# Kernel optimization log

Measured on AMD Instinct MI355X. Metric: run time of the kernel, lower is better.

The kernel has to match this reference:

```python
import jax, jax.numpy as jnp
import numpy as np

NUM_GRAPHS = 128
EPS = 1e-5


def _instance_norm(x, seg):
    # per-graph (segment) normalization over rows, per channel; affine=False (PyG default)
    ones = jnp.ones((x.shape[0],), x.dtype)
    cnt = jnp.maximum(jax.ops.segment_sum(ones, seg, num_segments=NUM_GRAPHS), 1.0)[:, None]
    mean = jax.ops.segment_sum(x, seg, num_segments=NUM_GRAPHS) / cnt
    ex2 = jax.ops.segment_sum(x * x, seg, num_segments=NUM_GRAPHS) / cnt
    var = jnp.maximum(ex2 - mean * mean, 0.0)
    return (x - mean[seg]) * jax.lax.rsqrt(var[seg] + EPS)


def setup_inputs() -> dict:
    key = jax.random.key(0)
    ks = jax.random.split(key, 6)
    N, E, H = 100_000, 1_600_000, 64
    emb = jax.random.normal(ks[0], (N, H), jnp.float32)
    edge_index = jax.random.randint(ks[1], (2, E), 0, N)
    batch = jnp.sort(jax.random.randint(ks[2], (N,), 0, NUM_GRAPHS))
    s = lambda fan: 1.0 / np.sqrt(fan)
    # MLP layers [2H, 4H, H, 1]
    W1 = jax.random.uniform(ks[3], (2 * H, 4 * H), jnp.float32, -s(2 * H), s(2 * H))
    b1 = jnp.zeros((4 * H,), jnp.float32)
    W2 = jax.random.uniform(ks[4], (4 * H, H), jnp.float32, -s(4 * H), s(4 * H))
    b2 = jnp.zeros((H,), jnp.float32)
    W3 = jax.random.uniform(ks[5], (H, 1), jnp.float32, -s(H), s(H))
    b3 = jnp.zeros((1,), jnp.float32)
    return dict(emb=emb, edge_index=edge_index, batch=batch,
                W1=W1, b1=b1, W2=W2, b2=b2, W3=W3, b3=b3)


def reference(emb, edge_index, batch, W1, b1, W2, b2, W3, b3):
    col, row = edge_index[0], edge_index[1]
    # edge-wise gather + concat: [E, 2H]
    f12 = jnp.concatenate([emb[col], emb[row]], axis=-1)
    seg = batch[col]  # graph id per edge
    h = jax.nn.relu(_instance_norm(f12 @ W1 + b1, seg))   # [E, 4H]
    h = jax.nn.relu(_instance_norm(h @ W2 + b2, seg))     # [E, H]
    att_log_logits = h @ W3 + b3                          # [E, 1]
    return att_log_logits
```

## Files before the change

kernel.cpp:

```cpp
#include <hip/hip_runtime.h>
#include <hip/hip_bf16.h>

#define NSEG 128
#define H64 64
#define C1 256
#define K1 128
#define C2 64
#define EPSV 1e-5f
#define NWG 256

typedef __attribute__((ext_vector_type(8))) short bf16x8;
typedef __attribute__((ext_vector_type(16))) float f32x16;
typedef __attribute__((ext_vector_type(4))) unsigned int u32x4;

struct BTrue  { static constexpr bool value = true; };
struct BFalse { static constexpr bool value = false; };

__device__ __forceinline__ unsigned short f2bf(float f){
  unsigned int x = __float_as_uint(f);
  x += 0x7fffu + ((x >> 16) & 1u);
  return (unsigned short)(x >> 16);
}
__device__ __forceinline__ float bf2f(unsigned short u){
  return __uint_as_float(((unsigned int)u) << 16);
}
__device__ __forceinline__ unsigned pkbf(float lo, float hi){
  unsigned r;
  asm("v_cvt_pk_bf16_f32 %0, %1, %2" : "=v"(r) : "v"(lo), "v"(hi));
  return r;
}
__device__ __forceinline__ bf16x8 mk8(unsigned a, unsigned b, unsigned c, unsigned d){
  u32x4 t = {a, b, c, d};
  return __builtin_bit_cast(bf16x8, t);
}
__device__ __forceinline__ int xcd_swz(int bid, int nwg){
  int q = nwg >> 3, r = nwg & 7;
  int x = bid & 7, o = bid >> 3;
  return (x < r ? x * (q + 1) : r * (q + 1) + (x - r) * q) + o;
}

__global__ void k_cvt_emb(const float* __restrict__ src, unsigned short* __restrict__ dst, int n4){
  int i = blockIdx.x * blockDim.x + threadIdx.x;
  if (i >= n4) return;
  float4 v = ((const float4*)src)[i];
  unsigned int a = (unsigned int)f2bf(v.x) | ((unsigned int)f2bf(v.y) << 16);
  unsigned int b = (unsigned int)f2bf(v.z) | ((unsigned int)f2bf(v.w) << 16);
  ((uint2*)dst)[i] = make_uint2(a, b);
}

__global__ void k_cvt_w(const float* __restrict__ W1, const float* __restrict__ W2,
                        unsigned short* __restrict__ W1T, unsigned short* __restrict__ W2T){
  int i = blockIdx.x * blockDim.x + threadIdx.x;
  if (i < C1 * K1){
    int c = i >> 7, k = i & 127;
    W1T[i] = f2bf(W1[k * C1 + c]);
  } else {
    int j = i - C1 * K1;
    if (j < C2 * C1){
      int c = j >> 8, k = j & 255;
      W2T[j] = f2bf(W2[k * C2 + c]);
    }
  }
}

__global__ void k_hist(const int* __restrict__ col, const int* __restrict__ batch,
                       int* __restrict__ segE, int* __restrict__ cnt, int E){
  __shared__ int h[NSEG];
  for (int i = threadIdx.x; i < NSEG; i += blockDim.x) h[i] = 0;
  __syncthreads();
  int stride = gridDim.x * blockDim.x;
  for (int e = blockIdx.x * blockDim.x + threadIdx.x; e < E; e += stride){
    int s = batch[col[e]];
    segE[e] = s;
    atomicAdd(&h[s], 1);
  }
  __syncthreads();
  for (int i = threadIdx.x; i < NSEG; i += blockDim.x)
    if (h[i]) atomicAdd(&cnt[i], h[i]);
}

__global__ void k_scan(const int* __restrict__ cnt, int* __restrict__ cursor,
                       float* __restrict__ cntf){
  if (threadIdx.x == 0){
    int acc = 0;
    for (int i = 0; i < NSEG; i++){ cursor[i] = acc; acc += cnt[i]; }
  }
  if (threadIdx.x < NSEG){
    int c = cnt[threadIdx.x];
    cntf[threadIdx.x] = (float)(c > 0 ? c : 1);
  }
}

__global__ void k_scatter(const int* __restrict__ segE, const int* __restrict__ ei,
                          int* __restrict__ cursor, int* __restrict__ perm,
                          int* __restrict__ segS, int* __restrict__ ecol, int* __restrict__ erow,
                          int E, int epb){
  __shared__ int h[NSEG];
  __shared__ int base[NSEG];
  int b0 = blockIdx.x * epb;
  int b1 = b0 + epb < E ? b0 + epb : E;
  for (int i = threadIdx.x; i < NSEG; i += blockDim.x) h[i] = 0;
  __syncthreads();
  for (int e = b0 + threadIdx.x; e < b1; e += blockDim.x) atomicAdd(&h[segE[e]], 1);
  __syncthreads();
  for (int i = threadIdx.x; i < NSEG; i += blockDim.x)
    base[i] = h[i] ? atomicAdd(&cursor[i], h[i]) : 0;
  __syncthreads();
  for (int i = threadIdx.x; i < NSEG; i += blockDim.x) h[i] = 0;
  __syncthreads();
  for (int e = b0 + threadIdx.x; e < b1; e += blockDim.x){
    int s = segE[e];
    int p = base[s] + atomicAdd(&h[s], 1);
    perm[p] = e; segS[p] = s;
    ecol[p] = ei[e]; erow[p] = ei[(size_t)E + e];
  }
}

__global__ void __launch_bounds__(1024, 4)
k_stats1(const unsigned short* __restrict__ ebf, const unsigned short* __restrict__ W1T,
         const int* __restrict__ ecol, const int* __restrict__ erow, const int* __restrict__ segS,
         float* __restrict__ sum1, float* __restrict__ sq1, int NWT, int E, int T)
{
  __shared__ __align__(16) char wl[65536];
  {
    #pragma unroll
    for (int j = 0; j < 4; j++){
      int i = threadIdx.x + j * 1024;
      int r = i >> 4, u = i & 15;
      u32x4 v = *(const u32x4*)(W1T + (size_t)r * K1 + u * 8);
      *(u32x4*)(wl + r * 256 + ((u ^ (r & 15)) << 4)) = v;
    }
  }
  __syncthreads();

  const int lane = threadIdx.x & 63, w = threadIdx.x >> 6;
  const int g = lane >> 5, l31 = lane & 31;
  const int bid = xcd_swz(blockIdx.x, NWG);
  const int wt0 = (bid * 16 + w) * T;
  float psum[8] = {0,0,0,0,0,0,0,0}, psq[8] = {0,0,0,0,0,0,0,0};
  int cur = -1;

  auto flush = [&](int seg){
    if (seg < 0) return;
    #pragma unroll
    for (int nt = 0; nt < 8; nt++){
      float sv = psum[nt] + __shfl_xor(psum[nt], 32);
      float qv = psq[nt]  + __shfl_xor(psq[nt], 32);
      if (lane < 32){
        atomicAdd(&sum1[seg * C1 + nt * 32 + l31], sv);
        atomicAdd(&sq1 [seg * C1 + nt * 32 + l31], qv);
      }
      psum[nt] = 0.f; psq[nt] = 0.f;
    }
  };

  auto ld3 = [&](int wt, int& a, int& r, int& s){
    int e = wt * 32 + l31;
    int ec = e < E ? e : E - 1;
    a = ecol[ec]; r = erow[ec]; s = segS[ec];
  };

  int cA, rA, sg;
  if (wt0 < NWT) ld3(wt0, cA, rA, sg);

  for (int it = 0; it < T; ++it){
    int wt = wt0 + it;
    if (wt >= NWT) break;
    const int p0 = wt * 32;
    int nA, nR, nS;
    const bool hv = (it + 1 < T) && (wt + 1 < NWT);
    if (hv) ld3(wt + 1, nA, nR, nS);

    bf16x8 fa[8];
    #pragma unroll
    for (int kk = 0; kk < 8; kk++){
      int off = (kk & 3) * 16 + g * 8;
      fa[kk] = *(const bf16x8*)(ebf + (size_t)(kk < 4 ? cA : rA) * H64 + off);
    }

    int sA = __builtin_amdgcn_readfirstlane(__shfl(sg, 0));
    int sB = __builtin_amdgcn_readfirstlane(__shfl(sg, 31));
    bool uni = (sA == sB) && (p0 + 32 <= E);
    if (uni && sA != cur){ flush(cur); cur = sA; }
    if (!uni){ flush(cur); cur = -1; }

    #pragma unroll 1
    for (int np = 0; np < 4; np++){
      const int nt0 = 2 * np, nt1 = 2 * np + 1;
      f32x16 a0, a1;
      #pragma unroll
      for (int r = 0; r < 16; r++){ a0[r] = 0.f; a1[r] = 0.f; }
      const int rw0 = nt0 * 32 + l31, rw1 = nt1 * 32 + l31;
      __builtin_amdgcn_s_setprio(1);
      #pragma unroll
      for (int kk = 0; kk < 8; kk++){
        bf16x8 b0 = *(const bf16x8*)(wl + rw0 * 256 + (((2 * kk + g) ^ (rw0 & 15)) << 4));
        bf16x8 b1 = *(const bf16x8*)(wl + rw1 * 256 + (((2 * kk + g) ^ (rw1 & 15)) << 4));
        a0 = __builtin_amdgcn_mfma_f32_32x32x16_bf16(fa[kk], b0, a0, 0, 0, 0);
        a1 = __builtin_amdgcn_mfma_f32_32x32x16_bf16(fa[kk], b1, a1, 0, 0, 0);
      }
      __builtin_amdgcn_s_setprio(0);
      if (uni){
        float t0 = 0.f, q0 = 0.f, t1 = 0.f, q1 = 0.f;
        #pragma unroll
        for (int r = 0; r < 16; r++){
          t0 += a0[r]; q0 += a0[r] * a0[r];
          t1 += a1[r]; q1 += a1[r] * a1[r];
        }
        psum[nt0] += t0; psq[nt0] += q0;
        psum[nt1] += t1; psq[nt1] += q1;
      } else {
        for (int s = sA; s <= sB; s++){
          float t0 = 0.f, q0 = 0.f, t1 = 0.f, q1 = 0.f;
          #pragma unroll
          for (int r = 0; r < 16; r++){
            int c = (r & 3) + 8 * (r >> 2) + 4 * g;
            bool ok = (__shfl(sg, c) == s) && (p0 + c < E);
            float v0 = ok ? a0[r] : 0.f;
            float v1 = ok ? a1[r] : 0.f;
            t0 += v0; q0 += v0 * v0;
            t1 += v1; q1 += v1 * v1;
          }
          float s0 = t0 + __shfl_xor(t0, 32);
          float qq0 = q0 + __shfl_xor(q0, 32);
          float s1 = t1 + __shfl_xor(t1, 32);
          float qq1 = q1 + __shfl_xor(q1, 32);
          if (lane < 32){
            atomicAdd(&sum1[s * C1 + nt0 * 32 + l31], s0);
            atomicAdd(&sq1 [s * C1 + nt0 * 32 + l31], qq0);
            atomicAdd(&sum1[s * C1 + nt1 * 32 + l31], s1);
            atomicAdd(&sq1 [s * C1 + nt1 * 32 + l31], qq1);
          }
        }
      }
    }
    if (hv){ cA = nA; rA = nR; sg = nS; }
  }
  flush(cur);
}

__global__ void k_fin(const float* __restrict__ sum, const float* __restrict__ sq,
                      const float* __restrict__ cntf,
                      float* __restrict__ sc, float* __restrict__ sh, int C){
  int i = blockIdx.x * blockDim.x + threadIdx.x;
  if (i >= NSEG * C) return;
  int s = i / C;
  float c = cntf[s];
  float m = sum[i] / c;
  float v = fmaxf(sq[i] / c - m * m, 0.f);
  float inv = rsqrtf(v + EPSV);
  sc[i] = inv;
  sh[i] = -m * inv;
}

template<int MODE>
__global__ void __launch_bounds__(1024, 4)
k_mid(const unsigned short* __restrict__ ebf, const unsigned short* __restrict__ W1T,
      const unsigned short* __restrict__ W2T,
      const int* __restrict__ ecol, const int* __restrict__ erow,
      const int* __restrict__ segS, const int* __restrict__ perm,
      const float* __restrict__ sc1, const float* __restrict__ sh1,
      float* __restrict__ sum2, float* __restrict__ sq2,
      unsigned int* __restrict__ y2u,
      const float* __restrict__ sc2, const float* __restrict__ sh2,
      const float* __restrict__ W3, const float* __restrict__ b3,
      float* __restrict__ out, int NWT, int E, int T)
{
  __shared__ __align__(16) char wl[98304];
  __shared__ __align__(16) float scsh[16][512];
  {
    #pragma unroll
    for (int j = 0; j < 4; j++){
      int i = threadIdx.x + j * 1024;
      int r = i >> 4, u = i & 15;
      u32x4 v = *(const u32x4*)(W1T + (size_t)r * K1 + u * 8);
      *(u32x4*)(wl + r * 256 + ((u ^ (r & 15)) << 4)) = v;
    }
    #pragma unroll
    for (int j = 0; j < 2; j++){
      int i = threadIdx.x + j * 1024;
      int r = i >> 5, u = i & 31;
      u32x4 v = *(const u32x4*)(W2T + (size_t)r * C1 + u * 8);
      *(u32x4*)(wl + 65536 + r * 512 + ((u ^ (r & 31)) << 4)) = v;
    }
  }
  __syncthreads();

  const int lane = threadIdx.x & 63, w = threadIdx.x >> 6;
  const int g = lane >> 5, l31 = lane & 31;
  const int bid = xcd_swz(blockIdx.x, NWG);
  const int wt0 = (bid * 16 + w) * T;

  float b3v = 0.f;
  if (MODE == 2) b3v = b3[0];
  int wseg = -1;

  auto body = [&](auto uni_c, const bf16x8* fbp, int sgn, f32x16* acc2){
    constexpr bool UNI = decltype(uni_c)::value;
    #pragma unroll 1
    for (int mt = 0; mt < 8; mt++){
      f32x16 a1;
      #pragma unroll
      for (int r = 0; r < 16; r++) a1[r] = 0.f;
      const int rw = mt * 32 + l31;
      __builtin_amdgcn_s_setprio(1);
      #pragma unroll
      for (int kk = 0; kk < 8; kk++){
        bf16x8 wa = *(const bf16x8*)(wl + rw * 256 + (((2 * kk + g) ^ (rw & 15)) << 4));
        a1 = __builtin_amdgcn_mfma_f32_32x32x16_bf16(wa, fbp[kk], a1, 0, 0, 0);
      }
      __builtin_amdgcn_s_setprio(0);
      unsigned pk_[8];
      #pragma unroll
      for (int rq = 0; rq < 4; rq++){
        float4 sc, sh;
        if constexpr (UNI){
          sc = *(const float4*)(&scsh[w][mt * 32 + rq * 8 + 4 * g]);
          sh = *(const float4*)(&scsh[w][256 + mt * 32 + rq * 8 + 4 * g]);
        } else {
          sc = *(const float4*)(sc1 + sgn * C1 + mt * 32 + rq * 8 + 4 * g);
          sh = *(const float4*)(sh1 + sgn * C1 + mt * 32 + rq * 8 + 4 * g);
        }
        float h0 = fmaxf(fmaf(a1[rq * 4 + 0], sc.x, sh.x), 0.f);
        float h1 = fmaxf(fmaf(a1[rq * 4 + 1], sc.y, sh.y), 0.f);
        float h2 = fmaxf(fmaf(a1[rq * 4 + 2], sc.z, sh.z), 0.f);
        float h3 = fmaxf(fmaf(a1[rq * 4 + 3], sc.w, sh.w), 0.f);
        pk_[rq * 2 + 0] = pkbf(h0, h1);
        pk_[rq * 2 + 1] = pkbf(h2, h3);
      }
      asm("v_permlane32_swap_b32 %0, %1" : "+v"(pk_[0]), "+v"(pk_[2]));
      asm("v_permlane32_swap_b32 %0, %1" : "+v"(pk_[1]), "+v"(pk_[3]));
      asm("v_permlane32_swap_b32 %0, %1" : "+v"(pk_[4]), "+v"(pk_[6]));
      asm("v_permlane32_swap_b32 %0, %1" : "+v"(pk_[5]), "+v"(pk_[7]));
      bf16x8 bf0 = mk8(pk_[0], pk_[1], pk_[2], pk_[3]);
      bf16x8 bf1 = mk8(pk_[4], pk_[5], pk_[6], pk_[7]);
      __builtin_amdgcn_s_setprio(1);
      #pragma unroll
      for (int ct = 0; ct < 2; ct++){
        int rb = ct * 32 + l31;
        bf16x8 wb0 = *(const bf16x8*)(wl + 65536 + rb * 512 + (((4 * mt + g) ^ (rb & 31)) << 4));
        bf16x8 wb1 = *(const bf16x8*)(wl + 65536 + rb * 512 + (((4 * mt + 2 + g) ^ (rb & 31)) << 4));
        acc2[ct] = __builtin_amdgcn_mfma_f32_32x32x16_bf16(wb0, bf0, acc2[ct], 0, 0, 0);
        acc2[ct] = __builtin_amdgcn_mfma_f32_32x32x16_bf16(wb1, bf1, acc2[ct], 0, 0, 0);
      }
      __builtin_amdgcn_s_setprio(0);
    }
  };

  auto ld3 = [&](int wt, int& a, int& r, int& s){
    int e = wt * 32 + l31;
    int ec = e < E ? e : E - 1;
    a = ecol[ec]; r = erow[ec]; s = segS[ec];
  };

  int cA, rA, sg;
  if (wt0 < NWT) ld3(wt0, cA, rA, sg);

  for (int it = 0; it < T; ++it){
    int wt = wt0 + it;
    if (wt >= NWT) break;
    const int p0 = wt * 32;
    int nA, nR, nS;
    const bool hv = (it + 1 < T) && (wt + 1 < NWT);
    if (hv) ld3(wt + 1, nA, nR, nS);

    int e0 = p0 + l31;
    bool v0 = e0 < E;

    bf16x8 fb[8];
    #pragma unroll
    for (int kk = 0; kk < 8; kk++){
      int off = (kk & 3) * 16 + g * 8;
      fb[kk] = *(const bf16x8*)(ebf + (size_t)(kk < 4 ? cA : rA) * H64 + off);
    }

    int sA = __builtin_amdgcn_readfirstlane(__shfl(sg, 0));
    int sB = __builtin_amdgcn_readfirstlane(__shfl(sg, 31));
    const bool uni = (sA == sB) && (p0 + 32 <= E);

    if (uni && sA != wseg){
      float4 s4 = *(const float4*)(sc1 + sA * C1 + lane * 4);
      float4 h4 = *(const float4*)(sh1 + sA * C1 + lane * 4);
      *(float4*)(&scsh[w][lane * 4]) = s4;
      *(float4*)(&scsh[w][256 + lane * 4]) = h4;
      wseg = sA;
    }

    f32x16 acc2[2];
    #pragma unroll
    for (int ct = 0; ct < 2; ct++)
      #pragma unroll
      for (int r = 0; r < 16; r++) acc2[ct][r] = 0.f;

    if (uni) body(BTrue{},  fb, sg, acc2);
    else     body(BFalse{}, fb, sg, acc2);

    if constexpr (MODE == 0){
      if (v0){
        unsigned* yp = y2u + (size_t)e0 * 32;
        #pragma unroll
        for (int ct = 0; ct < 2; ct++)
          #pragma unroll
          for (int rq = 0; rq < 4; rq++){
            uint2 pv;
            pv.x = pkbf(acc2[ct][rq * 4 + 0], acc2[ct][rq * 4 + 1]);
            pv.y = pkbf(acc2[ct][rq * 4 + 2], acc2[ct][rq * 4 + 3]);
            *(uint2*)(yp + ct * 16 + rq * 4 + 2 * g) = pv;
          }
      }
    } else if constexpr (MODE == 1){
      for (int s = sA; s <= sB; s++){
        #pragma unroll
        for (int ct = 0; ct < 2; ct++)
          #pragma unroll
          for (int r = 0; r < 16; r++){
            float x = (v0 && sg == s) ? acc2[ct][r] : 0.f;
            float vs = x, vq = x * x;
            #pragma unroll
            for (int off = 1; off < 32; off <<= 1){
              vs += __shfl_xor(vs, off);
              vq += __shfl_xor(vq, off);
            }
            if (l31 == 0){
              int c2 = ct * 32 + (r & 3) + 8 * (r >> 2) + 4 * g;
              atomicAdd(&sum2[s * C2 + c2], vs);
              atomicAdd(&sq2 [s * C2 + c2], vq);
            }
          }
      }
    } else {
      float acc = 0.f;
      #pragma unroll
      for (int ct = 0; ct < 2; ct++)
        #pragma unroll
        for (int rq = 0; rq < 4; rq++){
          float4 sc = *(const float4*)(sc2 + sg * C2 + ct * 32 + rq * 8 + 4 * g);
          float4 sh = *(const float4*)(sh2 + sg * C2 + ct * 32 + rq * 8 + 4 * g);
          float4 wq = *(const float4*)(W3 + ct * 32 + rq * 8 + 4 * g);
          acc = fmaf(fmaxf(fmaf(acc2[ct][rq * 4 + 0], sc.x, sh.x), 0.f), wq.x, acc);
          acc = fmaf(fmaxf(fmaf(acc2[ct][rq * 4 + 1], sc.y, sh.y), 0.f), wq.y, acc);
          acc = fmaf(fmaxf(fmaf(acc2[ct][rq * 4 + 2], sc.z, sh.z), 0.f), wq.z, acc);
          acc = fmaf(fmaxf(fmaf(acc2[ct][rq * 4 + 3], sc.w, sh.w), 0.f), wq.w, acc);
        }
      acc += __shfl_xor(acc, 32);
      if (g == 0 && v0) out[perm[e0]] = acc + b3v;
    }
    if (hv){ cA = nA; rA = nR; sg = nS; }
  }
}

__global__ void k_stats2(const unsigned int* __restrict__ y2u, const int* __restrict__ segS,
                         float* __restrict__ sum2, float* __restrict__ sq2, int E)
{
  const int cp = threadIdx.x & 31;
  const int es = threadIdx.x >> 5;
  int chunk = (E + gridDim.x - 1) / gridDim.x;
  int eb = blockIdx.x * chunk;
  int ee = eb + chunk < E ? eb + chunk : E;
  float s0 = 0.f, s1 = 0.f, q0 = 0.f, q1 = 0.f;
  int cur = -1;
  for (int e = eb + es; e < ee; e += 8){
    int sg = segS[e];
    unsigned v = y2u[(size_t)e * 32 + cp];
    float f0 = bf2f((unsigned short)(v & 0xffff));
    float f1 = bf2f((unsigned short)(v >> 16));
    if (sg != cur){
      if (cur >= 0){
        atomicAdd(&sum2[cur * C2 + 2 * cp], s0);
        atomicAdd(&sum2[cur * C2 + 2 * cp + 1], s1);
        atomicAdd(&sq2 [cur * C2 + 2 * cp], q0);
        atomicAdd(&sq2 [cur * C2 + 2 * cp + 1], q1);
      }
      s0 = s1 = q0 = q1 = 0.f; cur = sg;
    }
    s0 += f0; s1 += f1; q0 += f0 * f0; q1 += f1 * f1;
  }
  if (cur >= 0){
    atomicAdd(&sum2[cur * C2 + 2 * cp], s0);
    atomicAdd(&sum2[cur * C2 + 2 * cp + 1], s1);
    atomicAdd(&sq2 [cur * C2 + 2 * cp], q0);
    atomicAdd(&sq2 [cur * C2 + 2 * cp + 1], q1);
  }
}

__global__ void k_out(const unsigned short* __restrict__ y2, const int* __restrict__ segS,
                      const int* __restrict__ perm, const float* __restrict__ sc2,
                      const float* __restrict__ sh2, const float* __restrict__ W3,
                      const float* __restrict__ b3, float* __restrict__ out, int E)
{
  const int lane = threadIdx.x & 63;
  const int wid = (blockIdx.x * blockDim.x + threadIdx.x) >> 6;
  const int nw = (gridDim.x * blockDim.x) >> 6;
  const int es = lane >> 3;
  const int cp = (lane & 7) * 8;
  float w3r[8];
  #pragma unroll
  for (int j = 0; j < 8; j++) w3r[j] = W3[cp + j];
  const float b3v = b3[0];
  for (long base = (long)wid * 8; base < E; base += (long)nw * 8){
    int pos = (int)base + es;
    float a = 0.f;
    if (pos < E){
      bf16x8 v = *(const bf16x8*)(y2 + (size_t)pos * C2 + cp);
      int s = segS[pos];
      const float* scp = sc2 + s * C2 + cp;
      const float* shp = sh2 + s * C2 + cp;
      #pragma unroll
      for (int j = 0; j < 8; j++){
        float hv = fmaxf(fmaf(bf2f((unsigned short)v[j]), scp[j], shp[j]), 0.f);
        a = fmaf(hv, w3r[j], a);
      }
    }
    a += __shfl_xor(a, 1); a += __shfl_xor(a, 2); a += __shfl_xor(a, 4);
    if ((lane & 7) == 0 && pos < E) out[perm[pos]] = a + b3v;
  }
}

extern "C" void kernel_launch(void* const* d_in, const int* in_sizes, int n_in,
                              void* d_out, int out_size, void* d_ws, size_t ws_size,
                              hipStream_t stream)
{
  const float* emb   = (const float*)d_in[0];
  const int*   ei    = (const int*)d_in[1];
  const int*   batch = (const int*)d_in[2];
  const float* W1    = (const float*)d_in[3];
  const float* W2    = (const float*)d_in[5];
  const float* W3    = (const float*)d_in[7];
  const float* b3    = (const float*)d_in[8];
  float* out = (float*)d_out;
  const int E = in_sizes[1] / 2;
  const int N = in_sizes[0] / H64;
  const int NWT = (E + 31) / 32;

  char* ws = (char*)d_ws;
  size_t o = 0;
  auto al = [&](size_t b){ size_t r = o; o = (o + b + 255) & ~((size_t)255); return r; };
  size_t o_ebf  = al((size_t)N * H64 * 2);
  size_t o_w1t  = al((size_t)C1 * K1 * 2);
  size_t o_w2t  = al((size_t)C2 * C1 * 2);
  size_t o_perm = al((size_t)E * 4);
  size_t o_segS = al((size_t)E * 4);
  size_t o_ecol = al((size_t)E * 4);
  size_t o_erow = al((size_t)E * 4);
  size_t o_cnt  = al(NSEG * 4);
  size_t o_cur  = al(NSEG * 4);
  size_t o_cntf = al(NSEG * 4);
  size_t o_sum1 = al((size_t)NSEG * C1 * 4);
  size_t o_sq1  = al((size_t)NSEG * C1 * 4);
  size_t o_sum2 = al((size_t)NSEG * C2 * 4);
  size_t o_sq2  = al((size_t)NSEG * C2 * 4);
  size_t o_sc1  = al((size_t)NSEG * C1 * 4);
  size_t o_sh1  = al((size_t)NSEG * C1 * 4);
  size_t o_sc2  = al((size_t)NSEG * C2 * 4);
  size_t o_sh2  = al((size_t)NSEG * C2 * 4);
  size_t o_segE = al((size_t)E * 4);
  size_t o_y2   = o_segE;
  size_t need_full = o_segE + (size_t)E * C2 * 2;
  const bool full = ws_size >= need_full;

  unsigned short* ebf = (unsigned short*)(ws + o_ebf);
  unsigned short* W1T = (unsigned short*)(ws + o_w1t);
  unsigned short* W2T = (unsigned short*)(ws + o_w2t);
  int* perm = (int*)(ws + o_perm);
  int* segS = (int*)(ws + o_segS);
  int* ecol = (int*)(ws + o_ecol);
  int* erow = (int*)(ws + o_erow);
  int* cnt  = (int*)(ws + o_cnt);
  int* curp = (int*)(ws + o_cur);
  float* cntf = (float*)(ws + o_cntf);
  float* sum1 = (float*)(ws + o_sum1);
  float* sq1  = (float*)(ws + o_sq1);
  float* sum2 = (float*)(ws + o_sum2);
  float* sq2  = (float*)(ws + o_sq2);
  float* sc1  = (float*)(ws + o_sc1);
  float* sh1  = (float*)(ws + o_sh1);
  float* sc2  = (float*)(ws + o_sc2);
  float* sh2  = (float*)(ws + o_sh2);
  int* segE = (int*)(ws + o_segE);
  unsigned int* y2u = (unsigned int*)(ws + o_y2);
  unsigned short* y2 = (unsigned short*)(ws + o_y2);

  hipMemsetAsync(ws + o_cnt, 0, o_sc1 - o_cnt, stream);

  k_cvt_emb<<<(N * H64 / 4 + 255) / 256, 256, 0, stream>>>(emb, ebf, N * H64 / 4);
  k_cvt_w<<<192, 256, 0, stream>>>(W1, W2, W1T, W2T);

  k_hist<<<2048, 256, 0, stream>>>(ei, batch, segE, cnt, E);
  k_scan<<<1, 128, 0, stream>>>(cnt, curp, cntf);
  const int epb = 2048;
  k_scatter<<<(E + epb - 1) / epb, 256, 0, stream>>>(segE, ei, curp, perm, segS, ecol, erow, E, epb);

  const int T = (NWT + NWG * 16 - 1) / (NWG * 16);
  k_stats1<<<NWG, 1024, 0, stream>>>(ebf, W1T, ecol, erow, segS, sum1, sq1, NWT, E, T);
  k_fin<<<(NSEG * C1) / 256, 256, 0, stream>>>(sum1, sq1, cntf, sc1, sh1, C1);

  if (full){
    k_mid<0><<<NWG, 1024, 0, stream>>>(ebf, W1T, W2T, ecol, erow, segS, perm,
        sc1, sh1, sum2, sq2, y2u, sc2, sh2, W3, b3, out, NWT, E, T);
    k_stats2<<<512, 256, 0, stream>>>(y2u, segS, sum2, sq2, E);
    k_fin<<<(NSEG * C2) / 256, 256, 0, stream>>>(sum2, sq2, cntf, sc2, sh2, C2);
    k_out<<<1024, 256, 0, stream>>>(y2, segS, perm, sc2, sh2, W3, b3, out, E);
  } else {
    k_mid<1><<<NWG, 1024, 0, stream>>>(ebf, W1T, W2T, ecol, erow, segS, perm,
        sc1, sh1, sum2, sq2, nullptr, sc2, sh2, W3, b3, out, NWT, E, T);
    k_fin<<<(NSEG * C2) / 256, 256, 0, stream>>>(sum2, sq2, cntf, sc2, sh2, C2);
    k_mid<2><<<NWG, 1024, 0, stream>>>(ebf, W1T, W2T, ecol, erow, segS, perm,
        sc1, sh1, sum2, sq2, nullptr, sc2, sh2, W3, b3, out, NWT, E, T);
  }
}
```

Measured before the change: 674.1 us.

## Fuse layer-2 stats into mid kernel and replace scattered output write with gather remap

Removes the separate k_stats2 pass by computing layer-2 sum/sumsq with wave shuffles and atomics inside k_mid<0>, alongside the bf16 y2 store. k_out now writes results in sorted order to a temp buffer, and a new k_remap kernel gathers them back to original edge order using an inverse permutation recorded in k_scatter. This trades a full reread of y2 and a scattered write for more shuffle/atomic work in the main kernel, an extra invp write, and one extra small kernel. Stats are now taken from fp32 accumulators rather than the bf16-rounded values.

```diff
diff --git a/kernel.cpp b/kernel.cpp
--- a/kernel.cpp
+++ b/kernel.cpp
@@ -94,7 +94,7 @@
 __global__ void k_scatter(const int* __restrict__ segE, const int* __restrict__ ei,
                           int* __restrict__ cursor, int* __restrict__ perm,
                           int* __restrict__ segS, int* __restrict__ ecol, int* __restrict__ erow,
-                          int E, int epb){
+                          int* __restrict__ invp, int E, int epb){
   __shared__ int h[NSEG];
   __shared__ int base[NSEG];
   int b0 = blockIdx.x * epb;
@@ -113,6 +113,7 @@
     int p = base[s] + atomicAdd(&h[s], 1);
     perm[p] = e; segS[p] = s;
     ecol[p] = ei[e]; erow[p] = ei[(size_t)E + e];
+    invp[e] = p;
   }
 }
 
@@ -408,6 +409,25 @@
             *(uint2*)(yp + ct * 16 + rq * 4 + 2 * g) = pv;
           }
       }
+      for (int s = sA; s <= sB; s++){
+        #pragma unroll
+        for (int ct = 0; ct < 2; ct++)
+          #pragma unroll
+          for (int r = 0; r < 16; r++){
+            float x = (v0 && sg == s) ? acc2[ct][r] : 0.f;
+            float vs = x, vq = x * x;
+            #pragma unroll
+            for (int off = 1; off < 32; off <<= 1){
+              vs += __shfl_xor(vs, off);
+              vq += __shfl_xor(vq, off);
+            }
+            if (l31 == 0){
+              int c2 = ct * 32 + (r & 3) + 8 * (r >> 2) + 4 * g;
+              atomicAdd(&sum2[s * C2 + c2], vs);
+              atomicAdd(&sq2 [s * C2 + c2], vq);
+            }
+          }
+      }
     } else if constexpr (MODE == 1){
       for (int s = sA; s <= sB; s++){
         #pragma unroll
@@ -449,44 +469,10 @@
   }
 }
 
-__global__ void k_stats2(const unsigned int* __restrict__ y2u, const int* __restrict__ segS,
-                         float* __restrict__ sum2, float* __restrict__ sq2, int E)
-{
-  const int cp = threadIdx.x & 31;
-  const int es = threadIdx.x >> 5;
-  int chunk = (E + gridDim.x - 1) / gridDim.x;
-  int eb = blockIdx.x * chunk;
-  int ee = eb + chunk < E ? eb + chunk : E;
-  float s0 = 0.f, s1 = 0.f, q0 = 0.f, q1 = 0.f;
-  int cur = -1;
-  for (int e = eb + es; e < ee; e += 8){
-    int sg = segS[e];
-    unsigned v = y2u[(size_t)e * 32 + cp];
-    float f0 = bf2f((unsigned short)(v & 0xffff));
-    float f1 = bf2f((unsigned short)(v >> 16));
-    if (sg != cur){
-      if (cur >= 0){
-        atomicAdd(&sum2[cur * C2 + 2 * cp], s0);
-        atomicAdd(&sum2[cur * C2 + 2 * cp + 1], s1);
-        atomicAdd(&sq2 [cur * C2 + 2 * cp], q0);
-        atomicAdd(&sq2 [cur * C2 + 2 * cp + 1], q1);
-      }
-      s0 = s1 = q0 = q1 = 0.f; cur = sg;
-    }
-    s0 += f0; s1 += f1; q0 += f0 * f0; q1 += f1 * f1;
-  }
-  if (cur >= 0){
-    atomicAdd(&sum2[cur * C2 + 2 * cp], s0);
-    atomicAdd(&sum2[cur * C2 + 2 * cp + 1], s1);
-    atomicAdd(&sq2 [cur * C2 + 2 * cp], q0);
-    atomicAdd(&sq2 [cur * C2 + 2 * cp + 1], q1);
-  }
-}
-
 __global__ void k_out(const unsigned short* __restrict__ y2, const int* __restrict__ segS,
-                      const int* __restrict__ perm, const float* __restrict__ sc2,
-                      const float* __restrict__ sh2, const float* __restrict__ W3,
-                      const float* __restrict__ b3, float* __restrict__ out, int E)
+                      const float* __restrict__ sc2, const float* __restrict__ sh2,
+                      const float* __restrict__ W3, const float* __restrict__ b3,
+                      float* __restrict__ tmp, int E)
 {
   const int lane = threadIdx.x & 63;
   const int wid = (blockIdx.x * blockDim.x + threadIdx.x) >> 6;
@@ -512,8 +498,16 @@
       }
     }
     a += __shfl_xor(a, 1); a += __shfl_xor(a, 2); a += __shfl_xor(a, 4);
-    if ((lane & 7) == 0 && pos < E) out[perm[pos]] = a + b3v;
-  }
+    if ((lane & 7) == 0 && pos < E) tmp[pos] = a + b3v;
+  }
+}
+
+__global__ void k_remap(const float* __restrict__ tmp, const int* __restrict__ invp,
+                        float* __restrict__ out, int E)
+{
+  int stride = gridDim.x * blockDim.x;
+  for (int e = blockIdx.x * blockDim.x + threadIdx.x; e < E; e += stride)
+    out[e] = tmp[invp[e]];
 }
 
 extern "C" void kernel_launch(void* const* d_in, const int* in_sizes, int n_in,
@@ -542,6 +536,7 @@
   size_t o_segS = al((size_t)E * 4);
   size_t o_ecol = al((size_t)E * 4);
   size_t o_erow = al((size_t)E * 4);
+  size_t o_invp = al((size_t)E * 4);
   size_t o_cnt  = al(NSEG * 4);
   size_t o_cur  = al(NSEG * 4);
   size_t o_cntf = al(NSEG * 4);
@@ -565,6 +560,7 @@
   int* segS = (int*)(ws + o_segS);
   int* ecol = (int*)(ws + o_ecol);
   int* erow = (int*)(ws + o_erow);
+  int* invp = (int*)(ws + o_invp);
   int* cnt  = (int*)(ws + o_cnt);
   int* curp = (int*)(ws + o_cur);
   float* cntf = (float*)(ws + o_cntf);
@@ -579,6 +575,7 @@
   int* segE = (int*)(ws + o_segE);
   unsigned int* y2u = (unsigned int*)(ws + o_y2);
   unsigned short* y2 = (unsigned short*)(ws + o_y2);
+  float* tmp = (float*)(ws + o_ecol);
 
   hipMemsetAsync(ws + o_cnt, 0, o_sc1 - o_cnt, stream);
 
@@ -588,7 +585,7 @@
   k_hist<<<2048, 256, 0, stream>>>(ei, batch, segE, cnt, E);
   k_scan<<<1, 128, 0, stream>>>(cnt, curp, cntf);
   const int epb = 2048;
-  k_scatter<<<(E + epb - 1) / epb, 256, 0, stream>>>(segE, ei, curp, perm, segS, ecol, erow, E, epb);
+  k_scatter<<<(E + epb - 1) / epb, 256, 0, stream>>>(segE, ei, curp, perm, segS, ecol, erow, invp, E, epb);
 
   const int T = (NWT + NWG * 16 - 1) / (NWG * 16);
   k_stats1<<<NWG, 1024, 0, stream>>>(ebf, W1T, ecol, erow, segS, sum1, sq1, NWT, E, T);
@@ -597,9 +594,9 @@
   if (full){
     k_mid<0><<<NWG, 1024, 0, stream>>>(ebf, W1T, W2T, ecol, erow, segS, perm,
         sc1, sh1, sum2, sq2, y2u, sc2, sh2, W3, b3, out, NWT, E, T);
-    k_stats2<<<512, 256, 0, stream>>>(y2u, segS, sum2, sq2, E);
     k_fin<<<(NSEG * C2) / 256, 256, 0, stream>>>(sum2, sq2, cntf, sc2, sh2, C2);
-    k_out<<<1024, 256, 0, stream>>>(y2, segS, perm, sc2, sh2, W3, b3, out, E);
+    k_out<<<1024, 256, 0, stream>>>(y2, segS, sc2, sh2, W3, b3, tmp, E);
+    k_remap<<<2048, 256, 0, stream>>>(tmp, invp, out, E);
   } else {
     k_mid<1><<<NWG, 1024, 0, stream>>>(ebf, W1T, W2T, ecol, erow, segS, perm,
         sc1, sh1, sum2, sq2, nullptr, sc2, sh2, W3, b3, out, NWT, E, T);
```

New measurement: 658.7 us. 1.02x faster.
